# Optimization experiments

Hardware: AMD Instinct MI355X
Metric: run time of the kernel (lower is better)

The kernel has to match this reference:

```python
import jax, jax.numpy as jnp
import numpy as np

# Dimensions (match init_kwargs / input_specs)
B, L, HID, NH, HD, PROJ, NL = 4, 1024, 512, 8, 64, 2048, 2
LN_EPS = 1e-5


def _layer_norm(x, g, b):
    m = x.mean(-1, keepdims=True)
    v = ((x - m) ** 2).mean(-1, keepdims=True)
    return (x - m) / jnp.sqrt(v + LN_EPS) * g + b


def setup_inputs() -> dict:
    key = jax.random.key(0)
    ks = jax.random.split(key, 8)
    layer_x = jax.random.normal(ks[0], (B, L, HID), jnp.float32)
    # causal attention mask (True = masked), as built by mask_reshape (triu(1))
    causal = jnp.triu(jnp.ones((L, L), bool), 1)
    full_mask = jnp.broadcast_to(causal[None], (B, L, L))
    mask_multiplier = jnp.ones((B, L, 1), jnp.float32)
    s = 0.02
    qkv_w = (jax.random.normal(ks[1], (NL, HID, 3 * NH * HD), jnp.float32) * s)
    qkv_b = jnp.zeros((NL, 3 * NH * HD), jnp.float32)
    o_w = jax.random.normal(ks[2], (NL, NH * HD, HID), jnp.float32) * s
    o_b = jnp.zeros((NL, HID), jnp.float32)
    ln1_g = jnp.ones((NL, HID), jnp.float32)
    ln1_b = jnp.zeros((NL, HID), jnp.float32)
    ff_w1 = jax.random.normal(ks[3], (NL, HID, PROJ), jnp.float32) * s
    ff_b1 = jnp.zeros((NL, PROJ), jnp.float32)
    ff_w2 = jax.random.normal(ks[4], (NL, PROJ, HID), jnp.float32) * s
    ff_b2 = jnp.zeros((NL, HID), jnp.float32)
    ln2_g = jnp.ones((NL, HID), jnp.float32)
    ln2_b = jnp.zeros((NL, HID), jnp.float32)
    bd_w = jax.random.normal(ks[5], (HID, 1), jnp.float32) * s
    bd_b = jnp.zeros((1,), jnp.float32)
    return dict(layer_x=layer_x, full_mask=full_mask, mask_multiplier=mask_multiplier,
                qkv_w=qkv_w, qkv_b=qkv_b, o_w=o_w, o_b=o_b,
                ln1_g=ln1_g, ln1_b=ln1_b, ff_w1=ff_w1, ff_b1=ff_b1,
                ff_w2=ff_w2, ff_b2=ff_b2, ln2_g=ln2_g, ln2_b=ln2_b,
                bd_w=bd_w, bd_b=bd_b)


def reference(layer_x, full_mask, mask_multiplier, qkv_w, qkv_b, o_w, o_b,
              ln1_g, ln1_b, ff_w1, ff_b1, ff_w2, ff_b2, ln2_g, ln2_b,
              bd_w, bd_b):
    scale = 1.0 / np.sqrt(HD)
    out = layer_x
    for i in range(NL):  # n_layers dense Transformer_Block's (pre_lnorm)
        h = _layer_norm(out, ln1_g[i], ln1_b[i])
        qkv = h @ qkv_w[i] + qkv_b[i]
        q, k, v = jnp.split(qkv, 3, axis=-1)
        q = q.reshape(B, L, NH, HD)
        k = k.reshape(B, L, NH, HD)
        v = v.reshape(B, L, NH, HD)
        scores = jnp.einsum('bqhd,bkhd->bhqk', q, k) * scale
        scores = jnp.where(full_mask[:, None], -1e9, scores)
        attn = jax.nn.softmax(scores, axis=-1)
        av = jnp.einsum('bhqk,bkhd->bqhd', attn, v).reshape(B, L, NH * HD)
        out = out + (av @ o_w[i] + o_b[i])
        # Residual_FF (pre_lnorm)
        h2 = _layer_norm(out, ln2_g[i], ln2_b[i])
        out = out + (jax.nn.relu(h2 @ ff_w1[i] + ff_b1[i]) @ ff_w2[i] + ff_b2[i])
    # BoundaryDecision: per-token keep probability -> hard boundary mask
    bd_prob = jax.nn.sigmoid(out @ bd_w + bd_b)          # (B, L, 1)
    new_mask_multiplier = (bd_prob > 0.5).astype(out.dtype)
    # mode == 'full': blend refined output with the layer input
    new_out = out * mask_multiplier + (1.0 - mask_multiplier) * layer_x
    return new_out, new_mask_multiplier
```

## Files before the change

kernel.cpp:

```cpp
#include <hip/hip_runtime.h>
#include <math.h>

#define BB 4
#define LL 1024
#define HID 512
#define NH 8
#define HD 64
#define PROJ 2048
#define NLAYER 2
#define TOK (BB*LL)
#define QKV3 (3*NH*HD)
#define LN_EPS 1e-5f
#define PSTRIDE ((size_t)TOK * HID)

#define WST     3145728
#define OFF_QKV 0
#define OFF_O   786432
#define OFF_FF1 1048576
#define OFF_FF2 2097152

typedef unsigned short u16;
typedef unsigned int u32;
typedef _Float16 f16;
typedef __attribute__((ext_vector_type(8))) _Float16 half8;
typedef __attribute__((ext_vector_type(4))) float f32x4;

#define MFMAH(a,b,c) __builtin_amdgcn_mfma_f32_16x16x32_f16(a, b, c, 0, 0, 0)

__device__ inline u16 f16_rne(float x) {
    union { f16 h; u16 u; } c; c.h = (f16)x; return c.u;
}

__device__ __forceinline__ void gl16(const u16* g, u16* l) {
    __builtin_amdgcn_global_load_lds(
        (const __attribute__((address_space(1))) unsigned int*)(g),
        (__attribute__((address_space(3))) unsigned int*)(l),
        16, 0, 0);
}

__device__ inline int xcd_swz(int orig, int nwg) {
    int q = nwg >> 3, r = nwg & 7;
    int xcd = orig & 7, idx = orig >> 3;
    return (xcd < r) ? (xcd * (q + 1) + idx)
                     : (r * (q + 1) + (xcd - r) * q + idx);
}

__device__ inline float wave_sum(float v) {
#pragma unroll
    for (int m = 32; m; m >>= 1) v += __shfl_xor(v, m, 64);
    return v;
}

template<int FOLD>
__global__ __launch_bounds__(256) void ln_kernel(
    float* __restrict__ x, const float* __restrict__ P,
    const float* __restrict__ g, const float* __restrict__ b,
    u16* __restrict__ y)
{
    __shared__ float red[4];
    int row = blockIdx.x;
    float* xr = x + (size_t)row * HID;
    int t = threadIdx.x;
    int lane = t & 63, wid = t >> 6;
    float v0 = xr[t], v1 = xr[t + 256];
    if (FOLD > 0) {
        size_t off = (size_t)row * HID + t;
#pragma unroll
        for (int z = 0; z < FOLD; ++z) {
            v0 += P[z * PSTRIDE + off];
            v1 += P[z * PSTRIDE + off + 256];
        }
        xr[t] = v0; xr[t + 256] = v1;
    }
    float s = wave_sum(v0 + v1);
    if (lane == 0) red[wid] = s;
    __syncthreads();
    float mean = (red[0] + red[1] + red[2] + red[3]) * (1.0f / HID);
    __syncthreads();
    float d0 = v0 - mean, d1 = v1 - mean;
    s = wave_sum(d0 * d0 + d1 * d1);
    if (lane == 0) red[wid] = s;
    __syncthreads();
    float var = (red[0] + red[1] + red[2] + red[3]) * (1.0f / HID);
    float rstd = rsqrtf(var + LN_EPS);
    size_t o = (size_t)row * HID;
    y[o + t]       = f16_rne(d0 * rstd * g[t] + b[t]);
    y[o + t + 256] = f16_rne(d1 * rstd * g[t + 256] + b[t + 256]);
}

__global__ __launch_bounds__(256) void wprep_all(
    const float* __restrict__ qkv_w, const float* __restrict__ o_w,
    const float* __restrict__ ff_w1, const float* __restrict__ ff_w2,
    u16* __restrict__ wt)
{
    __shared__ float tile[32][33];
    int bid = blockIdx.x;
    int l = bid / 3072, rem = bid % 3072;
    const float* W; u16* T; int K, N, bx, by;
    if (rem < 768) {
        W = qkv_w + (size_t)l * HID * QKV3;
        T = wt + (size_t)l * WST + OFF_QKV;
        K = HID; N = QKV3; bx = rem % 48; by = rem / 48;
    } else if (rem < 1024) {
        int r2 = rem - 768;
        W = o_w + (size_t)l * HID * HID;
        T = wt + (size_t)l * WST + OFF_O;
        K = HID; N = HID; bx = r2 & 15; by = r2 >> 4;
    } else if (rem < 2048) {
        int r3 = rem - 1024;
        W = ff_w1 + (size_t)l * HID * PROJ;
        T = wt + (size_t)l * WST + OFF_FF1;
        K = HID; N = PROJ; bx = r3 & 63; by = r3 >> 6;
    } else {
        int r4 = rem - 2048;
        W = ff_w2 + (size_t)l * PROJ * HID;
        T = wt + (size_t)l * WST + OFF_FF2;
        K = PROJ; N = HID; bx = r4 & 15; by = r4 >> 4;
    }
    int tx = threadIdx.x & 31, ty = threadIdx.x >> 5;
    int k0 = by * 32, n0 = bx * 32;
#pragma unroll
    for (int r = 0; r < 32; r += 8)
        tile[ty + r][tx] = W[(size_t)(k0 + ty + r) * N + n0 + tx];
    __syncthreads();
#pragma unroll
    for (int r = 0; r < 32; r += 8) {
        float v = tile[tx][ty + r];
        T[(size_t)(n0 + ty + r) * K + k0 + tx] = f16_rne(v);
    }
}

template<int MODE, int SK>
__global__ __launch_bounds__(256) void gemm9(
    const u16* __restrict__ A, const u16* __restrict__ B,
    const float* __restrict__ bias, float* __restrict__ Cf,
    u16* __restrict__ Ch, u16* __restrict__ Cq, u16* __restrict__ Ck,
    u16* __restrict__ Cv, int M, int N, int K)
{
    __shared__ u16 sm[(128 + 64) * 64];
    int tid = threadIdx.x;
    int w = tid >> 6, lane = tid & 63;
    int hi = lane >> 4, lo16 = lane & 15;
    int wr = w >> 1, wc = w & 1;

    int gx = gridDim.x, nwg = gx * gridDim.y;
    int swz = xcd_swz(blockIdx.y * gx + blockIdx.x, nwg);
    int row0 = (swz / gx) * 128, col0 = (swz % gx) * 64;

    int kchunk = K / SK;
    int kbeg = blockIdx.z * kchunk;
    int nt = kchunk / 64;

    int srow = lane >> 3;
    int gcol = ((lane & 7) ^ srow) * 8;

    f32x4 acc[4][2] = {};

    for (int t = 0; t < nt; ++t) {
        int k0 = kbeg + t * 64;
        __syncthreads();
#pragma unroll
        for (int c = 0; c < 4; ++c) {
            int r0 = w * 32 + c * 8;
            gl16(A + (size_t)(row0 + r0 + srow) * K + k0 + gcol, &sm[r0 * 64]);
        }
#pragma unroll
        for (int c = 0; c < 2; ++c) {
            int r0 = w * 16 + c * 8;
            gl16(B + (size_t)(col0 + r0 + srow) * K + k0 + gcol,
                 &sm[8192 + r0 * 64]);
        }
        __syncthreads();

        half8 af[4][2], bf[2][2];
#pragma unroll
        for (int m = 0; m < 4; ++m) {
            int row = wr * 64 + m * 16 + lo16;
#pragma unroll
            for (int ks = 0; ks < 2; ++ks)
                af[m][ks] = *(const half8*)
                    &sm[row * 64 + (((ks * 4 + hi) ^ (row & 7)) * 8)];
        }
#pragma unroll
        for (int n = 0; n < 2; ++n) {
            int row = wc * 32 + n * 16 + lo16;
#pragma unroll
            for (int ks = 0; ks < 2; ++ks)
                bf[n][ks] = *(const half8*)
                    &sm[8192 + row * 64 + (((ks * 4 + hi) ^ (row & 7)) * 8)];
        }
#pragma unroll
        for (int m = 0; m < 4; ++m)
#pragma unroll
            for (int n = 0; n < 2; ++n)
#pragma unroll
                for (int ks = 0; ks < 2; ++ks)
                    acc[m][n] = MFMAH(af[m][ks], bf[n][ks], acc[m][n]);
    }

    size_t zoff = (size_t)blockIdx.z * M * N;
#pragma unroll
    for (int n = 0; n < 2; ++n) {
        int c = col0 + wc * 32 + n * 16 + lo16;
        float bv = (SK == 1 || blockIdx.z == 0) ? bias[c] : 0.0f;
#pragma unroll
        for (int m = 0; m < 4; ++m) {
            int rbase = row0 + wr * 64 + m * 16 + hi * 4;
#pragma unroll
            for (int r = 0; r < 4; ++r) {
                float x = acc[m][n][r] + bv;
                size_t idx = (size_t)(rbase + r) * N + c;
                if (MODE == 0) {
                    Ch[idx] = f16_rne(x);
                } else if (MODE == 1) {
                    Cf[zoff + idx] = x;
                } else if (MODE == 2) {
                    Ch[idx] = f16_rne(fmaxf(x, 0.0f));
                } else {
                    int tok = rbase + r;
                    int bbv = tok >> 10, tloc = tok & 1023;
                    if (c < HID) {
                        Cq[(((size_t)(bbv * NH + (c >> 6)) * LL + tloc) * HD)
                           + (c & 63)] = f16_rne(x * 0.125f);
                    } else if (c < 2 * HID) {
                        int cc = c - HID;
                        Ck[(((size_t)(bbv * NH + (cc >> 6)) * LL + tloc) * HD)
                           + (cc & 63)] = f16_rne(x);
                    } else {
                        int cc = c - 2 * HID;
                        Cv[(((size_t)(bbv * NH + (cc >> 6)) * HD + (cc & 63)) * LL)
                           + tloc] = f16_rne(x);
                    }
                }
            }
        }
    }
}

__global__ __launch_bounds__(256) void attn7(
    const u16* __restrict__ qP, const u16* __restrict__ kP,
    const u16* __restrict__ vT, u16* __restrict__ avh)
{
    __shared__ u16 Ks[64 * 64];
    __shared__ u16 Vt[64 * 64];
    __shared__ u16 Pl[4][1024];

    int gid = xcd_swz(blockIdx.x, gridDim.x);
    int qt = gid & 15;
    int bh = gid >> 4;
    int bb = bh >> 3, h = bh & 7;
    int tid = threadIdx.x;
    int w = tid >> 6, lane = tid & 63, hi = lane >> 4, lo16 = lane & 15;

    const u16* qsrc = qP + ((size_t)bh * LL + qt * 64 + w * 16 + lo16) * HD;
    half8 qf0 = *(const half8*)(qsrc + hi * 8);
    half8 qf1 = *(const half8*)(qsrc + 32 + hi * 8);

    const u16* kbase = kP + (size_t)bh * LL * HD;
    const u16* vbase = vT + (size_t)bh * HD * LL;

    half8 onesf;
#pragma unroll
    for (int j = 0; j < 8; ++j) onesf[j] = (f16)1.0f;

    f32x4 o[4] = {};
    f32x4 lacc = {};

    int srow8 = lane >> 3;
    int pc = lane & 7;

    for (int kt = 0; kt <= qt; ++kt) {
        __syncthreads();
#pragma unroll
        for (int c = 0; c < 2; ++c) {
            int r = w * 16 + c * 8 + srow8;
            int lc = (pc ^ (r & 7)) * 8;
            gl16(kbase + (size_t)(kt * 64 + r) * HD + lc, &Ks[(w * 16 + c * 8) * 64]);
            gl16(vbase + (size_t)r * LL + kt * 64 + lc, &Vt[(w * 16 + c * 8) * 64]);
        }
        __syncthreads();

        bool diag = (kt == qt);
#pragma unroll
        for (int n = 0; n < 4; ++n) {
            int kl = n * 16 + lo16;
            if (diag && n > w) {
#pragma unroll
                for (int r = 0; r < 4; ++r) {
                    int ql = hi * 4 + r;
                    u32 off = ((u32)(ql * 128 + kl * 2)) ^ ((ql & 7) << 4);
                    *(u16*)((char*)Pl[w] + off) = 0;
                }
                continue;
            }
            int tl = n * 16 + lo16;
            half8 kf0 = *(const half8*)&Ks[tl * 64 + ((hi ^ (tl & 7)) * 8)];
            half8 kf1 = *(const half8*)&Ks[tl * 64 + (((4 + hi) ^ (tl & 7)) * 8)];
            f32x4 z = {};
            z = MFMAH(qf0, kf0, z);
            z = MFMAH(qf1, kf1, z);
            if (diag && n == w) {
#pragma unroll
                for (int r = 0; r < 4; ++r)
                    if (lo16 > hi * 4 + r) z[r] = -1e30f;
            }
#pragma unroll
            for (int r = 0; r < 4; ++r) {
                float p = __expf(z[r] - 4.0f);
                int ql = hi * 4 + r;
                u32 off = ((u32)(ql * 128 + kl * 2)) ^ ((ql & 7) << 4);
                *(u16*)((char*)Pl[w] + off) = f16_rne(p);
            }
        }
        int cmax = diag ? (w >> 1) : 1;
#pragma unroll
        for (int c = 0; c < 2; ++c) {
            if (c > cmax) break;
            u32 off = ((u32)(lo16 * 128 + c * 64 + hi * 16)) ^ ((lo16 & 7) << 4);
            half8 pa = *(const half8*)((char*)Pl[w] + off);
            lacc = MFMAH(pa, onesf, lacc);
#pragma unroll
            for (int n = 0; n < 4; ++n) {
                int tl = n * 16 + lo16;
                half8 vb = *(const half8*)
                    &Vt[tl * 64 + (((c * 4 + hi) ^ (tl & 7)) * 8)];
                o[n] = MFMAH(pa, vb, o[n]);
            }
        }
    }

#pragma unroll
    for (int r = 0; r < 4; ++r) {
        float inv = 1.0f / lacc[r];
        int tokg = bb * LL + qt * 64 + w * 16 + hi * 4 + r;
#pragma unroll
        for (int n = 0; n < 4; ++n) {
            int d = n * 16 + lo16;
            avh[(size_t)tokg * (NH * HD) + h * HD + d] = f16_rne(o[n][r] * inv);
        }
    }
}

template<int FOLD>
__global__ __launch_bounds__(64) void bd_kernel(
    const float* __restrict__ outb, const float* __restrict__ P,
    const float* __restrict__ layer_x, const float* __restrict__ mm,
    const float* __restrict__ bd_w, const float* __restrict__ bd_b,
    float* __restrict__ d_out)
{
    int t = blockIdx.x;
    int lane = threadIdx.x;
    const float* orow = outb + (size_t)t * HID;
    float mmv = mm[t];
    const float* xrow = layer_x + (size_t)t * HID;
    float* yrow = d_out + (size_t)t * HID;
    float dot = 0.0f;
#pragma unroll
    for (int i = 0; i < 8; ++i) {
        int c = lane + 64 * i;
        float v = orow[c];
        if (FOLD > 0) {
            size_t off = (size_t)t * HID + c;
#pragma unroll
            for (int z = 0; z < FOLD; ++z) v += P[z * PSTRIDE + off];
        }
        dot += v * bd_w[c];
        yrow[c] = v * mmv + (1.0f - mmv) * xrow[c];
    }
    dot = wave_sum(dot);
    if (lane == 0) {
        float z = dot + bd_b[0];
        d_out[(size_t)TOK * HID + t] = (z > 0.0f) ? 1.0f : 0.0f;
    }
}

extern "C" void kernel_launch(void* const* d_in, const int* in_sizes, int n_in,
                              void* d_out, int out_size, void* d_ws, size_t ws_size,
                              hipStream_t stream) {
    const float* layer_x = (const float*)d_in[0];
    const float* mm      = (const float*)d_in[2];
    const float* qkv_w   = (const float*)d_in[3];
    const float* qkv_b   = (const float*)d_in[4];
    const float* o_w     = (const float*)d_in[5];
    const float* o_b     = (const float*)d_in[6];
    const float* ln1_g   = (const float*)d_in[7];
    const float* ln1_b   = (const float*)d_in[8];
    const float* ff_w1   = (const float*)d_in[9];
    const float* ff_b1   = (const float*)d_in[10];
    const float* ff_w2   = (const float*)d_in[11];
    const float* ff_b2   = (const float*)d_in[12];
    const float* ln2_g   = (const float*)d_in[13];
    const float* ln2_b   = (const float*)d_in[14];
    const float* bd_w    = (const float*)d_in[15];
    const float* bd_b    = (const float*)d_in[16];

    char* base = (char*)d_ws;
    float* buf_out = (float*)base;
    u16* hbuf = (u16*)(base + 8388608);
    u16* av   = (u16*)(base + 12582912);
    u16* big  = (u16*)(base + 16777216);
    u16* wt   = (u16*)(base + 33554432);
    float* part = (float*)(base + 46137344);
    u16* vTb  = (u16*)(base + 79691776);
    size_t need = 83886080;
    if (ws_size < need) return;
    u16* qPb  = big;
    u16* kPb  = big + 2097152;
    u16* tbuf = big;

    wprep_all<<<6144, 256, 0, stream>>>(qkv_w, o_w, ff_w1, ff_w2, wt);

    hipMemcpyAsync(buf_out, layer_x, (size_t)TOK * HID * sizeof(float),
                   hipMemcpyDeviceToDevice, stream);

    for (int l = 0; l < NLAYER; ++l) {
        size_t wb = (size_t)l * WST;
        if (l == 0)
            ln_kernel<0><<<TOK, 256, 0, stream>>>(
                buf_out, nullptr, ln1_g, ln1_b, hbuf);
        else
            ln_kernel<4><<<TOK, 256, 0, stream>>>(
                buf_out, part, ln1_g + (size_t)l * HID,
                ln1_b + (size_t)l * HID, hbuf);
        gemm9<3, 1><<<dim3(QKV3 / 64, TOK / 128, 1), 256, 0, stream>>>(
            hbuf, wt + wb + OFF_QKV, qkv_b + (size_t)l * QKV3,
            nullptr, nullptr, qPb, kPb, vTb, TOK, QKV3, HID);
        attn7<<<BB * NH * (LL / 64), 256, 0, stream>>>(qPb, kPb, vTb, av);
        gemm9<1, 2><<<dim3(HID / 64, TOK / 128, 2), 256, 0, stream>>>(
            av, wt + wb + OFF_O, o_b + (size_t)l * HID,
            part, nullptr, nullptr, nullptr, nullptr, TOK, HID, NH * HD);
        ln_kernel<2><<<TOK, 256, 0, stream>>>(
            buf_out, part, ln2_g + (size_t)l * HID,
            ln2_b + (size_t)l * HID, hbuf);
        gemm9<2, 1><<<dim3(PROJ / 64, TOK / 128, 1), 256, 0, stream>>>(
            hbuf, wt + wb + OFF_FF1, ff_b1 + (size_t)l * PROJ,
            nullptr, tbuf, nullptr, nullptr, nullptr, TOK, PROJ, HID);
        gemm9<1, 4><<<dim3(HID / 64, TOK / 128, 4), 256, 0, stream>>>(
            tbuf, wt + wb + OFF_FF2, ff_b2 + (size_t)l * HID,
            part, nullptr, nullptr, nullptr, nullptr, TOK, HID, PROJ);
    }

    bd_kernel<4><<<TOK, 64, 0, stream>>>(buf_out, part, layer_x, mm,
                                         bd_w, bd_b, (float*)d_out);
}
```

Baseline: 222.6 us.

## Load two KV tiles per barrier in attention and halve FF2 split-K

The attention kernel now stages two 64-row K/V tiles into double-sized shared buffers per sync pair and processes both before the next barrier, halving the number of barrier rounds and load phases. Separately, the FF2 GEMM split-K factor drops from 4 to 2, with the following layernorm and boundary kernels summing two partial buffers instead of four. This lowers partial-sum traffic and reduction work but gives the FF2 GEMM fewer blocks and a longer K loop per block. The larger shared memory footprint may reduce attention occupancy.

After: 219.7 us. No clear change (-1.3%).

```diff
diff --git a/kernel.cpp b/kernel.cpp
--- a/kernel.cpp
+++ b/kernel.cpp
@@ -237,12 +237,12 @@
     }
 }
 
-__global__ __launch_bounds__(256) void attn7(
+__global__ __launch_bounds__(256) void attn8(
     const u16* __restrict__ qP, const u16* __restrict__ kP,
     const u16* __restrict__ vT, u16* __restrict__ avh)
 {
-    __shared__ u16 Ks[64 * 64];
-    __shared__ u16 Vt[64 * 64];
+    __shared__ u16 Ks[2][64 * 64];
+    __shared__ u16 Vt[2][64 * 64];
     __shared__ u16 Pl[4][1024];
 
     int gid = xcd_swz(blockIdx.x, gridDim.x);
@@ -269,62 +269,71 @@
     int srow8 = lane >> 3;
     int pc = lane & 7;
 
-    for (int kt = 0; kt <= qt; ++kt) {
+    for (int g0 = 0; g0 <= qt; g0 += 2) {
         __syncthreads();
 #pragma unroll
-        for (int c = 0; c < 2; ++c) {
-            int r = w * 16 + c * 8 + srow8;
-            int lc = (pc ^ (r & 7)) * 8;
-            gl16(kbase + (size_t)(kt * 64 + r) * HD + lc, &Ks[(w * 16 + c * 8) * 64]);
-            gl16(vbase + (size_t)r * LL + kt * 64 + lc, &Vt[(w * 16 + c * 8) * 64]);
-        }
+        for (int s = 0; s < 2; ++s)
+#pragma unroll
+            for (int c = 0; c < 2; ++c) {
+                int r = w * 16 + c * 8 + srow8;
+                int lc = (pc ^ (r & 7)) * 8;
+                gl16(kbase + (size_t)((g0 + s) * 64 + r) * HD + lc,
+                     &Ks[s][(w * 16 + c * 8) * 64]);
+                gl16(vbase + (size_t)r * LL + (g0 + s) * 64 + lc,
+                     &Vt[s][(w * 16 + c * 8) * 64]);
+            }
         __syncthreads();
 
-        bool diag = (kt == qt);
-#pragma unroll
-        for (int n = 0; n < 4; ++n) {
-            int kl = n * 16 + lo16;
-            if (diag && n > w) {
+#pragma unroll
+        for (int s = 0; s < 2; ++s) {
+            int g = g0 + s;
+            if (g > qt) break;
+            bool diag = (g == qt);
+#pragma unroll
+            for (int n = 0; n < 4; ++n) {
+                int kl = n * 16 + lo16;
+                if (diag && n > w) {
+#pragma unroll
+                    for (int r = 0; r < 4; ++r) {
+                        int ql = hi * 4 + r;
+                        u32 off = ((u32)(ql * 128 + kl * 2)) ^ ((ql & 7) << 4);
+                        *(u16*)((char*)Pl[w] + off) = 0;
+                    }
+                    continue;
+                }
+                int tl = n * 16 + lo16;
+                half8 kf0 = *(const half8*)&Ks[s][tl * 64 + ((hi ^ (tl & 7)) * 8)];
+                half8 kf1 = *(const half8*)&Ks[s][tl * 64 + (((4 + hi) ^ (tl & 7)) * 8)];
+                f32x4 z = {};
+                z = MFMAH(qf0, kf0, z);
+                z = MFMAH(qf1, kf1, z);
+                if (diag && n == w) {
+#pragma unroll
+                    for (int r = 0; r < 4; ++r)
+                        if (lo16 > hi * 4 + r) z[r] = -1e30f;
+                }
 #pragma unroll
                 for (int r = 0; r < 4; ++r) {
+                    float p = __expf(z[r] - 4.0f);
                     int ql = hi * 4 + r;
                     u32 off = ((u32)(ql * 128 + kl * 2)) ^ ((ql & 7) << 4);
-                    *(u16*)((char*)Pl[w] + off) = 0;
+                    *(u16*)((char*)Pl[w] + off) = f16_rne(p);
                 }
-                continue;
             }
-            int tl = n * 16 + lo16;
-            half8 kf0 = *(const half8*)&Ks[tl * 64 + ((hi ^ (tl & 7)) * 8)];
-            half8 kf1 = *(const half8*)&Ks[tl * 64 + (((4 + hi) ^ (tl & 7)) * 8)];
-            f32x4 z = {};
-            z = MFMAH(qf0, kf0, z);
-            z = MFMAH(qf1, kf1, z);
-            if (diag && n == w) {
-#pragma unroll
-                for (int r = 0; r < 4; ++r)
-                    if (lo16 > hi * 4 + r) z[r] = -1e30f;
-            }
-#pragma unroll
-            for (int r = 0; r < 4; ++r) {
-                float p = __expf(z[r] - 4.0f);
-                int ql = hi * 4 + r;
-                u32 off = ((u32)(ql * 128 + kl * 2)) ^ ((ql & 7) << 4);
-                *(u16*)((char*)Pl[w] + off) = f16_rne(p);
-            }
-        }
-        int cmax = diag ? (w >> 1) : 1;
-#pragma unroll
-        for (int c = 0; c < 2; ++c) {
-            if (c > cmax) break;
-            u32 off = ((u32)(lo16 * 128 + c * 64 + hi * 16)) ^ ((lo16 & 7) << 4);
-            half8 pa = *(const half8*)((char*)Pl[w] + off);
-            lacc = MFMAH(pa, onesf, lacc);
-#pragma unroll
-            for (int n = 0; n < 4; ++n) {
-                int tl = n * 16 + lo16;
-                half8 vb = *(const half8*)
-                    &Vt[tl * 64 + (((c * 4 + hi) ^ (tl & 7)) * 8)];
-                o[n] = MFMAH(pa, vb, o[n]);
+            int cmax = diag ? (w >> 1) : 1;
+#pragma unroll
+            for (int c = 0; c < 2; ++c) {
+                if (c > cmax) break;
+                u32 off = ((u32)(lo16 * 128 + c * 64 + hi * 16)) ^ ((lo16 & 7) << 4);
+                half8 pa = *(const half8*)((char*)Pl[w] + off);
+                lacc = MFMAH(pa, onesf, lacc);
+#pragma unroll
+                for (int n = 0; n < 4; ++n) {
+                    int tl = n * 16 + lo16;
+                    half8 vb = *(const half8*)
+                        &Vt[s][tl * 64 + (((c * 4 + hi) ^ (tl & 7)) * 8)];
+                    o[n] = MFMAH(pa, vb, o[n]);
+                }
             }
         }
     }
@@ -419,13 +428,13 @@
             ln_kernel<0><<<TOK, 256, 0, stream>>>(
                 buf_out, nullptr, ln1_g, ln1_b, hbuf);
         else
-            ln_kernel<4><<<TOK, 256, 0, stream>>>(
+            ln_kernel<2><<<TOK, 256, 0, stream>>>(
                 buf_out, part, ln1_g + (size_t)l * HID,
                 ln1_b + (size_t)l * HID, hbuf);
         gemm9<3, 1><<<dim3(QKV3 / 64, TOK / 128, 1), 256, 0, stream>>>(
             hbuf, wt + wb + OFF_QKV, qkv_b + (size_t)l * QKV3,
             nullptr, nullptr, qPb, kPb, vTb, TOK, QKV3, HID);
-        attn7<<<BB * NH * (LL / 64), 256, 0, stream>>>(qPb, kPb, vTb, av);
+        attn8<<<BB * NH * (LL / 64), 256, 0, stream>>>(qPb, kPb, vTb, av);
         gemm9<1, 2><<<dim3(HID / 64, TOK / 128, 2), 256, 0, stream>>>(
             av, wt + wb + OFF_O, o_b + (size_t)l * HID,
             part, nullptr, nullptr, nullptr, nullptr, TOK, HID, NH * HD);
@@ -435,11 +444,11 @@
         gemm9<2, 1><<<dim3(PROJ / 64, TOK / 128, 1), 256, 0, stream>>>(
             hbuf, wt + wb + OFF_FF1, ff_b1 + (size_t)l * PROJ,
             nullptr, tbuf, nullptr, nullptr, nullptr, TOK, PROJ, HID);
-        gemm9<1, 4><<<dim3(HID / 64, TOK / 128, 4), 256, 0, stream>>>(
+        gemm9<1, 2><<<dim3(HID / 64, TOK / 128, 2), 256, 0, stream>>>(
             tbuf, wt + wb + OFF_FF2, ff_b2 + (size_t)l * HID,
             part, nullptr, nullptr, nullptr, nullptr, TOK, HID, PROJ);
     }
 
-    bd_kernel<4><<<TOK, 64, 0, stream>>>(buf_out, part, layer_x, mm,
+    bd_kernel<2><<<TOK, 64, 0, stream>>>(buf_out, part, layer_x, mm,
                                          bd_w, bd_b, (float*)d_out);
 }
```
